# Performance work log

Hardware: AMD Instinct MI355X
Metric: run time of the kernel (lower is better)

## Reference

```python
import jax, jax.numpy as jnp
import numpy as np

V_THRESH = 0.3

@jax.custom_vjp
def spike(x):
    return (x > 0).astype(x.dtype)

def _spike_fwd(x):
    return spike(x), x

def _spike_bwd(x, g):
    # rectangular straight-through surrogate gradient (pass grad where |x| < 0.5)
    return (g * (jnp.abs(x) < 0.5).astype(g.dtype),)

spike.defvjp(_spike_fwd, _spike_bwd)


def setup_inputs() -> dict:
    key = jax.random.key(0)
    B, T, H = 128, 2048, 128
    k1, = jax.random.split(key, 1)
    x_seq = jax.random.normal(k1, (B, T, H), dtype=jnp.float32)
    v0 = jnp.zeros((B, H), dtype=jnp.float32)
    z0 = jnp.zeros((B, H), dtype=jnp.float32)
    decay_raw = jnp.zeros((H,), dtype=jnp.float32)  # nn.initializers.constant(0.0)
    return {"x_seq": x_seq, "v0": v0, "z0": z0, "decay_raw": decay_raw}


def reference(x_seq, v0, z0, decay_raw):
    # LIF recurrence: v_t = v_{t-1} * decay * (1 - z_{t-1}) + x_t ; z_t = spike(v_t - v_thresh)
    decay = jax.nn.sigmoid(decay_raw)  # (H,)

    def step(carry, x_t):
        v, z = carry
        v = v * decay * (1.0 - z) + x_t
        z_out = spike(v - V_THRESH)
        return (v, z_out), z_out

    x_tb = jnp.swapaxes(x_seq, 0, 1)  # [T, B, H] for lax.scan over time
    (_, _), spk_tb = jax.lax.scan(step, (v0, z0), x_tb)
    return jnp.swapaxes(spk_tb, 0, 1)  # [B, T, H]
```

## Files before the change

### kernel.cpp

```cpp
#include <hip/hip_runtime.h>
#include <math.h>


constexpr int Bdim = 128;
constexpr int Tdim = 2048;
constexpr int Hdim = 128;
constexpr int HW   = 64;
constexpr int Ut   = 64;
constexpr int NT   = Tdim / Ut;
constexpr int NX   = 6;
constexpr int NZ   = 3;
constexpr int NLOAD = 6;
constexpr float VTH = 0.3f;

__device__ __forceinline__ void lgkm_fence() {
    asm volatile("s_waitcnt lgkmcnt(0)" ::: "memory");
}

__global__ __launch_bounds__(512) void lif_kernel(
    const float* __restrict__ x,
    const float* __restrict__ v0,
    const float* __restrict__ z0,
    const float* __restrict__ decay_raw,
    float* __restrict__ out)
{
    __shared__ float xbuf[NX][Ut][HW];
    __shared__ float zbuf[NZ][Ut][HW];
    __shared__ int   flags[NT + 8];

    volatile int* vf = (volatile int*)flags;

    const int tid  = threadIdx.x;
    const int wave = tid >> 6;
    const int lane = tid & 63;
    const int blk  = blockIdx.x;
    const int b    = blk >> 1;
    const int h0   = (blk & 1) * HW;

    for (int i = tid; i < NT + 8; i += 512) flags[i] = 0;
    __syncthreads();

    const float* xbase = x   + (size_t)b * Tdim * Hdim + h0;
    float*       obase = out + (size_t)b * Tdim * Hdim + h0;
    const int r_sub = lane >> 4;
    const int c_sub = (lane & 15) * 4;
    const int sub   = r_sub * Hdim + c_sub;

    if (wave >= 1 && wave <= NLOAD) {
        for (int k = wave - 1; k < NT; k += NLOAD) {
            while (vf[NT] < k - NX + 1) __builtin_amdgcn_s_sleep(2);
            const float* g = xbase + (size_t)k * Ut * Hdim + sub;
            float4 tmp[16];
            #pragma unroll
            for (int j = 0; j < 16; ++j)
                tmp[j] = *(const float4*)(g + (size_t)(4 * j) * Hdim);
            const int xb = k % NX;
            #pragma unroll
            for (int j = 0; j < 16; ++j)
                *(float4*)&xbuf[xb][4 * j + r_sub][c_sub] = tmp[j];
            lgkm_fence();
            if (lane == 0) vf[k] = 1;
        }
    } else if (wave == 0) {
        const float decay = 1.0f / (1.0f + expf(-decay_raw[h0 + lane]));
        float v = v0[b * Hdim + h0 + lane];
        float z = z0[b * Hdim + h0 + lane];

        for (int k = 0; k < NT; ++k) {
            while (vf[k] == 0)           __builtin_amdgcn_s_sleep(1);
            while (vf[NT + 2] < k - NZ + 1) __builtin_amdgcn_s_sleep(1);
            const int xb = k % NX, zb = k % NZ;
            #pragma unroll 16
            for (int t = 0; t < Ut; ++t) {
                const float xv = xbuf[xb][t][lane];
                const float s  = v * decay + xv;
                v = (z > 0.5f) ? xv : s;
                z = (v > VTH) ? 1.0f : 0.0f;
                zbuf[zb][t][lane] = z;
            }
            lgkm_fence();
            if (lane == 0) { vf[NT + 1] = k + 1; vf[NT] = k + 1; }
        }
    } else {
        for (int k = 0; k < NT; ++k) {
            while (vf[NT + 1] < k + 1) __builtin_amdgcn_s_sleep(1);
            const int zb = k % NZ;
            float4 vv[16];
            #pragma unroll
            for (int s = 0; s < 16; ++s)
                vv[s] = *(const float4*)&zbuf[zb][4 * s + r_sub][c_sub];
            lgkm_fence();
            if (lane == 0) vf[NT + 2] = k + 1;
            float* op = obase + (size_t)k * Ut * Hdim + sub;
            #pragma unroll
            for (int s = 0; s < 16; ++s)
                *(float4*)(op + (size_t)(4 * s) * Hdim) = vv[s];
        }
    }
}

extern "C" void kernel_launch(void* const* d_in, const int* in_sizes, int n_in,
                              void* d_out, int out_size, void* d_ws, size_t ws_size,
                              hipStream_t stream) {
    const float* x         = (const float*)d_in[0];
    const float* v0        = (const float*)d_in[1];
    const float* z0        = (const float*)d_in[2];
    const float* decay_raw = (const float*)d_in[3];
    float* out = (float*)d_out;

    lif_kernel<<<Bdim * Hdim / HW, 512, 0, stream>>>(x, v0, z0, decay_raw, out);
}
```

Measured before the change: 254.7 us.

## Buffer spikes as LDS bitmasks and write output after the recurrence

The dedicated store wave and the small float spike ring buffer are replaced by packing each timestep's spike into 32-bit masks, keeping the whole sequence in LDS (16KB per block). After the recurrence finishes, a block barrier lets all eight waves expand the bits to floats and write the output. The x-prefetch ring grows to 8 slots with 7 loader waves, and each block sleeps for a short time that depends on its index, to spread out the initial load requests. This drops the compute-to-store handshake and frees the input stream from competing stores, but output writes no longer overlap the serial recurrence and now happen as a burst at the end.

Measured after the change: 246.5 us. 3.2% less time.

```diff
diff --git a/kernel.cpp b/kernel.cpp
--- a/kernel.cpp
+++ b/kernel.cpp
@@ -8,9 +8,8 @@
 constexpr int HW   = 64;
 constexpr int Ut   = 64;
 constexpr int NT   = Tdim / Ut;
-constexpr int NX   = 6;
-constexpr int NZ   = 3;
-constexpr int NLOAD = 6;
+constexpr int NX   = 8;
+constexpr int NLOAD = 7;
 constexpr float VTH = 0.3f;
 
 __device__ __forceinline__ void lgkm_fence() {
@@ -24,9 +23,9 @@
     const float* __restrict__ decay_raw,
     float* __restrict__ out)
 {
-    __shared__ float xbuf[NX][Ut][HW];
-    __shared__ float zbuf[NZ][Ut][HW];
-    __shared__ int   flags[NT + 8];
+    __shared__ float    xbuf[NX][Ut][HW];
+    __shared__ unsigned zbits[Tdim / 32][HW];
+    __shared__ int      flags[NT + 4];
 
     volatile int* vf = (volatile int*)flags;
 
@@ -37,8 +36,10 @@
     const int b    = blk >> 1;
     const int h0   = (blk & 1) * HW;
 
-    for (int i = tid; i < NT + 8; i += 512) flags[i] = 0;
+    for (int i = tid; i < NT + 4; i += 512) flags[i] = 0;
     __syncthreads();
+
+    for (int i = 0; i < (blk & 3); ++i) __builtin_amdgcn_s_sleep(16);
 
     const float* xbase = x   + (size_t)b * Tdim * Hdim + h0;
     float*       obase = out + (size_t)b * Tdim * Hdim + h0;
@@ -46,9 +47,9 @@
     const int c_sub = (lane & 15) * 4;
     const int sub   = r_sub * Hdim + c_sub;
 
-    if (wave >= 1 && wave <= NLOAD) {
+    if (wave >= 1) {
         for (int k = wave - 1; k < NT; k += NLOAD) {
-            while (vf[NT] < k - NX + 1) __builtin_amdgcn_s_sleep(2);
+            while (vf[NT] < k - (NX - 1)) __builtin_amdgcn_s_sleep(2);
             const float* g = xbase + (size_t)k * Ut * Hdim + sub;
             float4 tmp[16];
             #pragma unroll
@@ -61,40 +62,43 @@
             lgkm_fence();
             if (lane == 0) vf[k] = 1;
         }
-    } else if (wave == 0) {
+    } else {
         const float decay = 1.0f / (1.0f + expf(-decay_raw[h0 + lane]));
         float v = v0[b * Hdim + h0 + lane];
         float z = z0[b * Hdim + h0 + lane];
 
         for (int k = 0; k < NT; ++k) {
-            while (vf[k] == 0)           __builtin_amdgcn_s_sleep(1);
-            while (vf[NT + 2] < k - NZ + 1) __builtin_amdgcn_s_sleep(1);
-            const int xb = k % NX, zb = k % NZ;
-            #pragma unroll 16
-            for (int t = 0; t < Ut; ++t) {
-                const float xv = xbuf[xb][t][lane];
-                const float s  = v * decay + xv;
-                v = (z > 0.5f) ? xv : s;
-                z = (v > VTH) ? 1.0f : 0.0f;
-                zbuf[zb][t][lane] = z;
+            while (vf[k] == 0) __builtin_amdgcn_s_sleep(1);
+            const int xb = k % NX;
+            #pragma unroll
+            for (int w32 = 0; w32 < Ut / 32; ++w32) {
+                unsigned mask = 0u;
+                #pragma unroll
+                for (int tb = 0; tb < 32; ++tb) {
+                    const int t = w32 * 32 + tb;
+                    const float xv = xbuf[xb][t][lane];
+                    const float s  = v * decay + xv;
+                    v = (z > 0.5f) ? xv : s;
+                    const bool sp = (v > VTH);
+                    z = sp ? 1.0f : 0.0f;
+                    mask |= (sp ? 1u : 0u) << tb;
+                }
+                zbits[k * (Ut / 32) + w32][lane] = mask;
             }
             lgkm_fence();
-            if (lane == 0) { vf[NT + 1] = k + 1; vf[NT] = k + 1; }
+            if (lane == 0) vf[NT] = k + 1;
         }
-    } else {
-        for (int k = 0; k < NT; ++k) {
-            while (vf[NT + 1] < k + 1) __builtin_amdgcn_s_sleep(1);
-            const int zb = k % NZ;
-            float4 vv[16];
-            #pragma unroll
-            for (int s = 0; s < 16; ++s)
-                vv[s] = *(const float4*)&zbuf[zb][4 * s + r_sub][c_sub];
-            lgkm_fence();
-            if (lane == 0) vf[NT + 2] = k + 1;
-            float* op = obase + (size_t)k * Ut * Hdim + sub;
-            #pragma unroll
-            for (int s = 0; s < 16; ++s)
-                *(float4*)(op + (size_t)(4 * s) * Hdim) = vv[s];
+    }
+
+    __syncthreads();
+
+    {
+        const int t0 = wave * (Tdim / 8);
+        #pragma unroll 8
+        for (int t = t0; t < t0 + Tdim / 8; ++t) {
+            const unsigned word = zbits[t >> 5][lane];
+            const float f = ((word >> (t & 31)) & 1u) ? 1.0f : 0.0f;
+            obase[(size_t)t * Hdim + lane] = f;
         }
     }
 }
```
